# Performance work log

Hardware: AMD Instinct MI355X
Metric: run time of the kernel (lower is better)

The kernel has to match this reference:

```python
import jax, jax.numpy as jnp
import numpy as np

EPS = 1e-5
PI = np.pi
HPK_SCL = 4.0  # args.hpk_scl

def _nan_to(y, rep):
    return jnp.where(jnp.isnan(y), rep, y)

def _chi(x):
    return _nan_to(1.0 / jnp.sqrt(1.0 + PI * jnp.tan(x + EPS) ** 2), 0.0)

def _E1(x, th):
    return _nan_to(jnp.exp(-(2.0 / PI) / jnp.tan(th + EPS) / jnp.tan(x + EPS)), 0.0)

def _E2(x, th):
    return _nan_to(jnp.exp(-(1.0 / PI) * (1.0 / jnp.tan(th + EPS)) ** 2 * (1.0 / jnp.tan(x + EPS)) ** 2), 0.0)

def _eta(x, th):
    y = _chi(th) * (jnp.cos(x) + jnp.sin(x) * jnp.tan(th + EPS) * (_E2(x, th) / (2.0 - _E1(x, th))))
    return _nan_to(y, 0.0)

def _f(phi):
    return _nan_to(jnp.exp(-2.0 * jnp.tan((phi + EPS) / 2.0)), 0.0)

def _mu_eff(i, e, phi, th):
    E1i, E1e = _E1(i, th), _E1(e, th)
    E2i, E2e = _E2(i, th), _E2(e, th)
    sp2 = jnp.sin(phi / 2.0) ** 2
    y1 = (E2e - sp2 * E2i) / (2.0 - E1e - phi / PI * E1i)
    y2 = (jnp.cos(phi) * E2i + sp2 * E2e) / (2.0 - E1i - phi / PI * E1e)
    y = jnp.where(i <= e, y1, y2)
    y = _chi(th) * (jnp.cos(e) + jnp.sin(e) * jnp.tan(th) * y)
    return _nan_to(y, jnp.cos(e))

def _mu0_eff(i, e, phi, th):
    E1i, E1e = _E1(i, th), _E1(e, th)
    E2i, E2e = _E2(i, th), _E2(e, th)
    sp2 = jnp.sin(phi / 2.0) ** 2
    y1 = (jnp.cos(phi) * E2e + sp2 * E2i) / (2.0 - E1e - phi / PI * E1i)
    y2 = (E2i - sp2 * E2e) / (2.0 - E1i - phi / PI * E1e)
    y = jnp.where(i <= e, y1, y2)
    y = _chi(th) * (jnp.cos(i) + jnp.sin(i) * jnp.tan(th) * y)
    return _nan_to(y, jnp.cos(i))

def _S(i, e, phi, th):
    ci, cv = jnp.cos(i), jnp.cos(e)
    mue = _mu_eff(i, e, phi, th)
    etai, etae = _eta(i, th), _eta(e, th)
    chit = _chi(th)
    ff = _f(phi)
    temp = mue / etae * (ci / etai) * chit
    y = jnp.where(i <= e,
                  temp / (1.0 - ff + ff * chit * (ci / etai)),
                  temp / (1.0 - ff + ff * chit * (cv / etae)))
    return _nan_to(y, 0.0)

def _HF(x, w):
    gamma = jnp.sqrt(1.0 - w)
    ro = (1.0 - gamma) / (1.0 + gamma)
    log = jnp.log(jnp.abs((1.0 + x) / x))
    tmp1 = 1.0 - w * x * (ro + (1.0 - 2.0 * ro * x) / 2.0 * log)
    return _nan_to(1.0 / tmp1, 1.0)

def _PF(x, b, c):
    b2 = b ** 2
    bx = b * x
    y = c * (1.0 - b2) / (jnp.power(1.0 - 2.0 * bx + b2, 1.5) + 1e-6)
    y = y + (1.0 - c) * (1.0 - b2) / (jnp.power(1.0 + 2.0 * bx + b2, 1.5) + 1e-6)
    return _nan_to(y, 0.0)

def _normalize(x):
    return x / (jnp.linalg.norm(x, axis=-1, keepdims=True) + 1e-8)

def setup_inputs() -> dict:
    N = 1048576
    key = jax.random.key(0)
    ks = jax.random.split(key, 9)
    normal = _normalize(jax.random.normal(ks[0], (N, 3), dtype=jnp.float32))
    l = _normalize(jax.random.normal(ks[1], (N, 3), dtype=jnp.float32))
    l = l * jnp.where(jnp.sum(l * normal, -1, keepdims=True) >= 0, 1.0, -1.0)  # upper hemisphere
    v = _normalize(jax.random.normal(ks[2], (N, 3), dtype=jnp.float32))
    v = v * jnp.where(jnp.sum(v * normal, -1, keepdims=True) >= 0, 1.0, -1.0)
    return {
        'pts2l': l[:, None, :],
        'pts2c': v,
        'normal': normal,
        'w': 0.05 + 0.9 * jax.random.uniform(ks[3], (N, 3), dtype=jnp.float32),
        'b': 0.8 * jax.random.uniform(ks[4], (N, 3), dtype=jnp.float32),
        'c': jax.random.uniform(ks[5], (N, 3), dtype=jnp.float32),
        'theta': 0.05 + 0.5 * jax.random.uniform(ks[6], (N,), dtype=jnp.float32),
        'h': 0.05 + 0.5 * jax.random.uniform(ks[7], (N, 1), dtype=jnp.float32),
        'B0': jax.random.uniform(ks[8], (N, 1), dtype=jnp.float32),
    }

def reference(pts2l, pts2c, normal, w, b, c, theta, h, B0):
    l = pts2l[:, 0, :]
    v = pts2c
    # angles (basic_func.calc_angles)
    ci = jnp.clip(jnp.sum(normal * l, -1), -1.0, 1.0)   # cos(incidence)
    sza = jnp.arccos(ci)
    si = jnp.sin(sza)
    cv = jnp.clip(jnp.sum(normal * v, -1), -1.0, 1.0)   # cos(view)
    vza = jnp.arccos(cv)
    sv = jnp.sin(vza)
    cg = jnp.clip(jnp.sum(l * v, -1), -1.0, 1.0)        # cos(phase)
    g = jnp.arccos(cg)
    cphi = jnp.clip((cg - ci * cv) / (si * sv + 1e-8), -1.0, 1.0)
    phi = jnp.arccos(cphi)                              # relative azimuth

    P = _PF(cg[:, None], b, c)                          # [N,3] phase function
    B = B0 / (1.0 + (1.0 / h) * jnp.tan(g / 2.0)[:, None]) + 1.0  # [N,1] opposition surge

    ci_e = _mu0_eff(sza, vza, phi, theta)               # roughness-corrected cosines
    cv_e = _mu_eff(sza, vza, phi, theta)
    Shad = _S(sza, vza, phi, theta)[:, None]            # [N,1] shadowing

    Hi = _HF(ci_e[:, None], w)                          # Chandrasekhar H functions
    Hv = _HF(cv_e[:, None], w)

    tmp1 = (ci_e / (ci_e + cv_e) / jnp.cos(sza))[:, None]
    tmp2 = P * B + Hi * Hv - 1.0
    brdf = w / HPK_SCL * tmp1 * tmp2 * Shad
    return brdf
```

## Files before the change

kernel.cpp:

```cpp
#include <hip/hip_runtime.h>


#define PIF  3.14159265358979323846f
#define EPSF 1e-5f

typedef float v2f __attribute__((ext_vector_type(2)));

__device__ __forceinline__ float rcp(float x)  { return __builtin_amdgcn_rcpf(x); }
__device__ __forceinline__ float rsq(float x)  { return __builtin_amdgcn_rsqf(x); }
__device__ __forceinline__ float sqf(float x)  { return __builtin_amdgcn_sqrtf(x); }
__device__ __forceinline__ float nz(float y, float r) { return (y != y) ? r : y; }
__device__ __forceinline__ float clamp1(float x) { return fminf(fmaxf(x, -1.0f), 1.0f); }
__device__ __forceinline__ float acos_poly(float x) {
    float a = fabsf(x);
    float r = sqf(1.0f - a) *
              (1.5707288f + a * (-0.2121144f + a * (0.0742610f + a * (-0.0187293f))));
    return (x >= 0.0f) ? r : (PIF - r);
}

__device__ __forceinline__ void hapke_point(
    float lx, float ly, float lz,
    float vx, float vy, float vz,
    float nx, float ny, float nzc,
    float th, float hh, float B0v,
    float w0, float w1, float w2,
    float b0, float b1, float b2,
    float c0, float c1, float c2,
    float outv[3])
{
    float ci  = clamp1(nx*lx + ny*ly + nzc*lz);
    float cvv = clamp1(nx*vx + ny*vy + nzc*vz);
    float cg  = clamp1(lx*vx + ly*vy + lz*vz);
    float si  = sqf(1.0f - ci*ci);
    float sv  = sqf(1.0f - cvv*cvv);
    float cphi = clamp1((cg - ci*cvv) * rcp(si*sv + 1e-8f));
    float phipi = acos_poly(cphi) * (1.0f / PIF);

    float ffu = (1.0f - cphi) * rcp(1.0f + cphi);
    float ff  = (cphi <= -1.0f) ? __builtin_inff() : __expf(-2.0f * sqf(ffu));

    float s = __sinf(th + EPSF), cth = __cosf(th + EPSF);
    float tt     = s * rcp(cth);
    float cot_th = cth * rcp(s);
    float cot_i  = ci * rcp(si);
    float cot_e  = cvv * rcp(sv);

    float E1i = nz(__expf(-(2.0f/PIF) * cot_th * cot_i), 0.0f);
    float E1e = nz(__expf(-(2.0f/PIF) * cot_th * cot_e), 0.0f);
    float ct2 = cot_th * cot_th;
    float E2i = nz(__expf(-(1.0f/PIF) * ct2 * cot_i*cot_i), 0.0f);
    float E2e = nz(__expf(-(1.0f/PIF) * ct2 * cot_e*cot_e), 0.0f);

    float chit = rsq(1.0f + PIF * tt * tt);
    float etai = nz(chit * (ci  + si * tt * (E2i * rcp(2.0f - E1i))), 0.0f);
    float etae = nz(chit * (cvv + sv * tt * (E2e * rcp(2.0f - E1e))), 0.0f);

    float sp2 = 0.5f * (1.0f - cphi);
    bool  ile = (ci >= cvv);
    float Ea  = ile ? E1e : E1i;
    float Eb  = ile ? E1i : E1e;
    float rd  = rcp(2.0f - Ea - phipi * Eb);
    float ymu  = (ile ? (E2e - sp2*E2i)      : (cphi*E2i + sp2*E2e)) * rd;
    float ymu0 = (ile ? (cphi*E2e + sp2*E2i) : (E2i - sp2*E2e)) * rd;
    float cv_e = nz(chit * (cvv + sv * tt * ymu ), cvv);
    float ci_e = nz(chit * (ci  + si * tt * ymu0), ci);

    float r_etai = rcp(etai), r_etae = rcp(etae);
    float ci_etai = ci * r_etai, cv_etae = cvv * r_etae;
    float temp = cv_e * r_etae * ci_etai * chit;
    float den  = 1.0f - ff + ff * chit * (ile ? ci_etai : cv_etae);
    float shad = nz(temp * rcp(den), 0.0f);

    float tg2 = sqf((1.0f - cg) * rcp(1.0f + cg));
    float B   = B0v * hh * rcp(hh + tg2) + 1.0f;
    float tmp1 = ci_e * rcp((ci_e + cv_e) * ci);

    float logi = 0.5f * __logf(fabsf((1.0f + ci_e) * rcp(ci_e)));
    float loge = 0.5f * __logf(fabsf((1.0f + cv_e) * rcp(cv_e)));

    const float wk3[3] = {w0, w1, w2};
    const float bk3[3] = {b0, b1, b2};
    const float ck3[3] = {c0, c1, c2};
    #pragma unroll
    for (int k = 0; k < 3; ++k) {
        float wk = wk3[k], bk = bk3[k], ck = ck3[k];
        float b2 = bk * bk, bx = bk * cg;
        float t1 = 1.0f - 2.0f*bx + b2;
        float t2 = 1.0f + 2.0f*bx + b2;
        float q1 = t1 * sqf(t1) + 1e-6f;
        float q2 = t2 * sqf(t2) + 1e-6f;
        float P  = (1.0f - b2) * (ck*q2 + (1.0f - ck)*q1) * rcp(q1*q2);
        float gamma = sqf(1.0f - wk);
        float ro = (1.0f - gamma) * rcp(1.0f + gamma);
        float Hi = nz(rcp(1.0f - wk*ci_e*(ro + (1.0f - 2.0f*ro*ci_e)*logi)), 1.0f);
        float Hv = nz(rcp(1.0f - wk*cv_e*(ro + (1.0f - 2.0f*ro*cv_e)*loge)), 1.0f);
        float tmp2 = P * B + Hi * Hv - 1.0f;
        outv[k] = wk * 0.25f * tmp1 * tmp2 * shad;
    }
}

__global__ __launch_bounds__(256, 4)
void hapke_kernel(const float* __restrict__ pts2l, const float* __restrict__ pts2c,
                  const float* __restrict__ normal, const float* __restrict__ w,
                  const float* __restrict__ b, const float* __restrict__ c,
                  const float* __restrict__ theta, const float* __restrict__ h,
                  const float* __restrict__ B0, float* __restrict__ out, int N)
{
    int t  = blockIdx.x * blockDim.x + threadIdx.x;
    int p0 = t * 2;
    if (p0 >= N) return;

    if (p0 + 1 < N) {
        const v2f* L2 = (const v2f*)pts2l;
        const v2f* V2 = (const v2f*)pts2c;
        const v2f* N2 = (const v2f*)normal;
        const v2f* W2 = (const v2f*)w;
        const v2f* Bb2 = (const v2f*)b;
        const v2f* C2 = (const v2f*)c;
        const v2f* T2 = (const v2f*)theta;
        const v2f* H2 = (const v2f*)h;
        const v2f* Z2 = (const v2f*)B0;

        int t3 = 3 * t;
        v2f la = L2[t3], lb = L2[t3+1], lc = L2[t3+2];
        v2f va = V2[t3], vb = V2[t3+1], vc = V2[t3+2];
        v2f na = N2[t3], nb = N2[t3+1], nc = N2[t3+2];
        v2f wa = W2[t3], wb = W2[t3+1], wc = W2[t3+2];
        v2f ba = Bb2[t3], bb = Bb2[t3+1], bc = Bb2[t3+2];
        v2f ca = C2[t3], cb = C2[t3+1], cc = C2[t3+2];
        v2f th2 = T2[t], h2 = H2[t], z2 = Z2[t];

        float oA[3], oB[3];
        hapke_point(la.x, la.y, lb.x,  va.x, va.y, vb.x,  na.x, na.y, nb.x,
                    th2.x, h2.x, z2.x,
                    wa.x, wa.y, wb.x,  ba.x, ba.y, bb.x,  ca.x, ca.y, cb.x, oA);
        hapke_point(lb.y, lc.x, lc.y,  vb.y, vc.x, vc.y,  nb.y, nc.x, nc.y,
                    th2.y, h2.y, z2.y,
                    wb.y, wc.x, wc.y,  bb.y, bc.x, bc.y,  cb.y, cc.x, cc.y, oB);

        v2f* O2 = (v2f*)out;
        v2f s0; s0.x = oA[0]; s0.y = oA[1];
        v2f s1; s1.x = oA[2]; s1.y = oB[0];
        v2f s2; s2.x = oB[1]; s2.y = oB[2];
        __builtin_nontemporal_store(s0, &O2[t3]);
        __builtin_nontemporal_store(s1, &O2[t3+1]);
        __builtin_nontemporal_store(s2, &O2[t3+2]);
    } else {
        int i3 = p0 * 3;
        float oA[3];
        hapke_point(pts2l[i3], pts2l[i3+1], pts2l[i3+2],
                    pts2c[i3], pts2c[i3+1], pts2c[i3+2],
                    normal[i3], normal[i3+1], normal[i3+2],
                    theta[p0], h[p0], B0[p0],
                    w[i3], w[i3+1], w[i3+2],
                    b[i3], b[i3+1], b[i3+2],
                    c[i3], c[i3+1], c[i3+2], oA);
        out[i3] = oA[0]; out[i3+1] = oA[1]; out[i3+2] = oA[2];
    }
}

extern "C" void kernel_launch(void* const* d_in, const int* in_sizes, int n_in,
                              void* d_out, int out_size, void* d_ws, size_t ws_size,
                              hipStream_t stream) {
    const float* pts2l  = (const float*)d_in[0];
    const float* pts2c  = (const float*)d_in[1];
    const float* normal = (const float*)d_in[2];
    const float* w      = (const float*)d_in[3];
    const float* b      = (const float*)d_in[4];
    const float* c      = (const float*)d_in[5];
    const float* theta  = (const float*)d_in[6];
    const float* h      = (const float*)d_in[7];
    const float* B0     = (const float*)d_in[8];
    float* out = (float*)d_out;

    int N = in_sizes[6];
    const int block = 256;
    int nthreads = (N + 1) / 2;
    int grid = (nthreads + block - 1) / block;
    hapke_kernel<<<grid, block, 0, stream>>>(pts2l, pts2c, normal, w, b, c,
                                             theta, h, B0, out, N);
}
```

Baseline: 123.3 us.

## Stage AoS inputs through LDS with float4 coalesced loads, one point per thread

Each block now loads the six 3-component input arrays for 256 points into shared memory with fully coalesced 16-byte vector loads, then each thread reads its own point's components from LDS. It replaces the earlier two-points-per-thread scheme that used 8-byte strided loads. The aim is better global-memory coalescing on a bandwidth-bound kernel. The cost is 18 KB of LDS per block, a block barrier, LDS bank conflicts from the stride-3 reads, and half as much work per thread, which lowers instruction-level parallelism.

```diff
diff --git a/kernel.cpp b/kernel.cpp
--- a/kernel.cpp
+++ b/kernel.cpp
@@ -4,7 +4,7 @@
 #define PIF  3.14159265358979323846f
 #define EPSF 1e-5f
 
-typedef float v2f __attribute__((ext_vector_type(2)));
+typedef float v4f __attribute__((ext_vector_type(4)));
 
 __device__ __forceinline__ float rcp(float x)  { return __builtin_amdgcn_rcpf(x); }
 __device__ __forceinline__ float rsq(float x)  { return __builtin_amdgcn_rsqf(x); }
@@ -99,6 +99,8 @@
     }
 }
 
+#define PTS 256
+
 __global__ __launch_bounds__(256, 4)
 void hapke_kernel(const float* __restrict__ pts2l, const float* __restrict__ pts2c,
                   const float* __restrict__ normal, const float* __restrict__ w,
@@ -106,56 +108,55 @@
                   const float* __restrict__ theta, const float* __restrict__ h,
                   const float* __restrict__ B0, float* __restrict__ out, int N)
 {
-    int t  = blockIdx.x * blockDim.x + threadIdx.x;
-    int p0 = t * 2;
-    if (p0 >= N) return;
+    __shared__ __align__(16) float sL[PTS*3];
+    __shared__ __align__(16) float sV[PTS*3];
+    __shared__ __align__(16) float sN[PTS*3];
+    __shared__ __align__(16) float sW[PTS*3];
+    __shared__ __align__(16) float sB[PTS*3];
+    __shared__ __align__(16) float sC[PTS*3];
 
-    if (p0 + 1 < N) {
-        const v2f* L2 = (const v2f*)pts2l;
-        const v2f* V2 = (const v2f*)pts2c;
-        const v2f* N2 = (const v2f*)normal;
-        const v2f* W2 = (const v2f*)w;
-        const v2f* Bb2 = (const v2f*)b;
-        const v2f* C2 = (const v2f*)c;
-        const v2f* T2 = (const v2f*)theta;
-        const v2f* H2 = (const v2f*)h;
-        const v2f* Z2 = (const v2f*)B0;
+    const int tid = threadIdx.x;
+    const int blockStart = blockIdx.x * PTS;
+    const int p = blockStart + tid;
 
-        int t3 = 3 * t;
-        v2f la = L2[t3], lb = L2[t3+1], lc = L2[t3+2];
-        v2f va = V2[t3], vb = V2[t3+1], vc = V2[t3+2];
-        v2f na = N2[t3], nb = N2[t3+1], nc = N2[t3+2];
-        v2f wa = W2[t3], wb = W2[t3+1], wc = W2[t3+2];
-        v2f ba = Bb2[t3], bb = Bb2[t3+1], bc = Bb2[t3+2];
-        v2f ca = C2[t3], cb = C2[t3+1], cc = C2[t3+2];
-        v2f th2 = T2[t], h2 = H2[t], z2 = Z2[t];
+    if (blockStart + PTS <= N) {
+        const int f4base = blockIdx.x * (PTS * 3 / 4);
+        if (tid < PTS * 3 / 4) {
+            ((v4f*)sL)[tid] = ((const v4f*)pts2l )[f4base + tid];
+            ((v4f*)sV)[tid] = ((const v4f*)pts2c )[f4base + tid];
+            ((v4f*)sN)[tid] = ((const v4f*)normal)[f4base + tid];
+            ((v4f*)sW)[tid] = ((const v4f*)w     )[f4base + tid];
+            ((v4f*)sB)[tid] = ((const v4f*)b     )[f4base + tid];
+            ((v4f*)sC)[tid] = ((const v4f*)c     )[f4base + tid];
+        }
+        float th = theta[p], hh = h[p], zz = B0[p];
+        __syncthreads();
 
-        float oA[3], oB[3];
-        hapke_point(la.x, la.y, lb.x,  va.x, va.y, vb.x,  na.x, na.y, nb.x,
-                    th2.x, h2.x, z2.x,
-                    wa.x, wa.y, wb.x,  ba.x, ba.y, bb.x,  ca.x, ca.y, cb.x, oA);
-        hapke_point(lb.y, lc.x, lc.y,  vb.y, vc.x, vc.y,  nb.y, nc.x, nc.y,
-                    th2.y, h2.y, z2.y,
-                    wb.y, wc.x, wc.y,  bb.y, bc.x, bc.y,  cb.y, cc.x, cc.y, oB);
+        const int t3 = tid * 3;
+        float o[3];
+        hapke_point(sL[t3], sL[t3+1], sL[t3+2],
+                    sV[t3], sV[t3+1], sV[t3+2],
+                    sN[t3], sN[t3+1], sN[t3+2],
+                    th, hh, zz,
+                    sW[t3], sW[t3+1], sW[t3+2],
+                    sB[t3], sB[t3+1], sB[t3+2],
+                    sC[t3], sC[t3+1], sC[t3+2], o);
 
-        v2f* O2 = (v2f*)out;
-        v2f s0; s0.x = oA[0]; s0.y = oA[1];
-        v2f s1; s1.x = oA[2]; s1.y = oB[0];
-        v2f s2; s2.x = oB[1]; s2.y = oB[2];
-        __builtin_nontemporal_store(s0, &O2[t3]);
-        __builtin_nontemporal_store(s1, &O2[t3+1]);
-        __builtin_nontemporal_store(s2, &O2[t3+2]);
-    } else {
-        int i3 = p0 * 3;
-        float oA[3];
+        const int i3 = p * 3;
+        __builtin_nontemporal_store(o[0], &out[i3]);
+        __builtin_nontemporal_store(o[1], &out[i3+1]);
+        __builtin_nontemporal_store(o[2], &out[i3+2]);
+    } else if (p < N) {
+        const int i3 = p * 3;
+        float o[3];
         hapke_point(pts2l[i3], pts2l[i3+1], pts2l[i3+2],
                     pts2c[i3], pts2c[i3+1], pts2c[i3+2],
                     normal[i3], normal[i3+1], normal[i3+2],
-                    theta[p0], h[p0], B0[p0],
+                    theta[p], h[p], B0[p],
                     w[i3], w[i3+1], w[i3+2],
                     b[i3], b[i3+1], b[i3+2],
-                    c[i3], c[i3+1], c[i3+2], oA);
-        out[i3] = oA[0]; out[i3+1] = oA[1]; out[i3+2] = oA[2];
+                    c[i3], c[i3+1], c[i3+2], o);
+        out[i3] = o[0]; out[i3+1] = o[1]; out[i3+2] = o[2];
     }
 }
 
@@ -175,8 +176,7 @@
 
     int N = in_sizes[6];
     const int block = 256;
-    int nthreads = (N + 1) / 2;
-    int grid = (nthreads + block - 1) / block;
+    int grid = (N + block - 1) / block;
     hapke_kernel<<<grid, block, 0, stream>>>(pts2l, pts2c, normal, w, b, c,
                                              theta, h, B0, out, N);
 }
```

After: 124.8 us. Within noise of the previous version (+1.2%).
